# Kernel optimization log

Measured on AMD Instinct MI355X. Metric: run time of the kernel, lower is better.

## Reference

```python
import jax, jax.numpy as jnp
import numpy as np


def _elu_plus_one(x):
    # F.elu(x) + 1 == exp(x) for x<0, x+1 for x>=0
    return jnp.where(x > 0, x + 1.0, jnp.exp(jnp.minimum(x, 0.0)))


def setup_inputs() -> dict:
    key = jax.random.key(0)
    kq, kk, kv = jax.random.split(key, 3)
    B, N, D = 16, 8192, 64
    q = jax.random.normal(kq, (B, N, D), dtype=jnp.float32)
    k = jax.random.normal(kk, (B, N, D), dtype=jnp.float32)
    v = jax.random.normal(kv, (B, N, D), dtype=jnp.float32)
    return {"q": q, "k": k, "v": v}


def reference(q, k, v):
    # linear attention with elu+1 feature map:
    # out = phi(q) @ (phi(k)^T @ v) / (D * N)
    qf = _elu_plus_one(q)          # [B, N, D]
    kf = _elu_plus_one(k)          # [B, N, D]
    kv = jnp.einsum('bnd,bne->bde', kf, v)   # [B, D, D] small intermediate
    denom = jnp.asarray(v.shape[-1] * v.shape[-2], dtype=v.dtype)
    out = jnp.einsum('bnd,bde->bne', qf, kv) / denom  # [B, N, D]
    return out
```

## Files before the change

### kernel.cpp

```cpp
#include <hip/hip_runtime.h>

#define B_ 16
#define N_ 8192
#define D_ 64

__device__ __forceinline__ float elu1(float x) {
    return x > 0.0f ? x + 1.0f : __expf(x);
}

__global__ __launch_bounds__(256, 4) void k1_partial(const float* __restrict__ kin,
                                                     const float* __restrict__ vin,
                                                     float* __restrict__ part,
                                                     int C, int R) {
    const int bid = blockIdx.x;
    const int b = bid / C, c = bid % C;
    const int w = threadIdx.x >> 6;
    const int lane = threadIdx.x & 63;
    const int dq = lane >> 3;
    const int eq = lane & 7;

    const int rows_per_wave = R >> 2;
    const size_t row0 = (size_t)b * N_ + (size_t)c * R + (size_t)w * rows_per_wave;
    const float* kbase = kin + row0 * D_ + 8 * dq;
    const float* vbase = vin + row0 * D_ + 8 * eq;

    float acc[8][8];
#pragma unroll
    for (int i = 0; i < 8; ++i)
#pragma unroll
        for (int jj = 0; jj < 8; ++jj) acc[i][jj] = 0.0f;

    for (int r = 0; r < rows_per_wave; r += 2) {
        const float4 ka0 = *(const float4*)(kbase + (size_t)(r + 0) * D_);
        const float4 kb0 = *(const float4*)(kbase + (size_t)(r + 0) * D_ + 4);
        const float4 va0 = *(const float4*)(vbase + (size_t)(r + 0) * D_);
        const float4 vb0 = *(const float4*)(vbase + (size_t)(r + 0) * D_ + 4);
        const float4 ka1 = *(const float4*)(kbase + (size_t)(r + 1) * D_);
        const float4 kb1 = *(const float4*)(kbase + (size_t)(r + 1) * D_ + 4);
        const float4 va1 = *(const float4*)(vbase + (size_t)(r + 1) * D_);
        const float4 vb1 = *(const float4*)(vbase + (size_t)(r + 1) * D_ + 4);

        const float kk0[8] = {elu1(ka0.x), elu1(ka0.y), elu1(ka0.z), elu1(ka0.w),
                              elu1(kb0.x), elu1(kb0.y), elu1(kb0.z), elu1(kb0.w)};
        const float vv0[8] = {va0.x, va0.y, va0.z, va0.w, vb0.x, vb0.y, vb0.z, vb0.w};
#pragma unroll
        for (int i = 0; i < 8; ++i)
#pragma unroll
            for (int jj = 0; jj < 8; ++jj)
                acc[i][jj] = __fmaf_rn(kk0[i], vv0[jj], acc[i][jj]);

        const float kk1[8] = {elu1(ka1.x), elu1(ka1.y), elu1(ka1.z), elu1(ka1.w),
                              elu1(kb1.x), elu1(kb1.y), elu1(kb1.z), elu1(kb1.w)};
        const float vv1[8] = {va1.x, va1.y, va1.z, va1.w, vb1.x, vb1.y, vb1.z, vb1.w};
#pragma unroll
        for (int i = 0; i < 8; ++i)
#pragma unroll
            for (int jj = 0; jj < 8; ++jj)
                acc[i][jj] = __fmaf_rn(kk1[i], vv1[jj], acc[i][jj]);
    }

    __shared__ float red[D_ * D_];
    for (int ww = 0; ww < 4; ++ww) {
        if (w == ww) {
#pragma unroll
            for (int i = 0; i < 8; ++i)
#pragma unroll
                for (int jq = 0; jq < 2; ++jq) {
                    float* p = &red[(8 * dq + i) * D_ + 8 * eq + 4 * jq];
                    if (ww == 0) {
                        float4 o = {acc[i][4 * jq + 0], acc[i][4 * jq + 1],
                                    acc[i][4 * jq + 2], acc[i][4 * jq + 3]};
                        *(float4*)p = o;
                    } else {
                        float4 cur = *(const float4*)p;
                        float4 o = {cur.x + acc[i][4 * jq + 0], cur.y + acc[i][4 * jq + 1],
                                    cur.z + acc[i][4 * jq + 2], cur.w + acc[i][4 * jq + 3]};
                        *(float4*)p = o;
                    }
                }
        }
        __syncthreads();
    }

    float4* pb = (float4*)(part + (size_t)bid * (D_ * D_));
    const float4* rp = (const float4*)red;
#pragma unroll
    for (int u = 0; u < 4; ++u)
        pb[threadIdx.x + 256 * u] = rp[threadIdx.x + 256 * u];
}

template <int TI>
__global__ __launch_bounds__(256) void k1_atomic(const float* __restrict__ kin,
                                                 const float* __restrict__ vin,
                                                 float* __restrict__ kv,
                                                 int C, int R) {
    const int bid = blockIdx.x;
    const int b = bid / C, c = bid % C;
    const size_t base = ((size_t)b * N_ + (size_t)c * R) * D_;
    const float4* kp = (const float4*)(kin + base);
    const float4* vp = (const float4*)(vin + base);

    __shared__ float lk[TI][D_];
    __shared__ float lv[TI][D_];

    const int tid = threadIdx.x;
    const int td = tid >> 4;
    const int te = tid & 15;

    float acc[4][4];
#pragma unroll
    for (int i = 0; i < 4; ++i)
#pragma unroll
        for (int j = 0; j < 4; ++j) acc[i][j] = 0.0f;

    const int ntiles = R / TI;
    for (int t = 0; t < ntiles; ++t) {
#pragma unroll
        for (int u = tid; u < TI * (D_ / 4); u += 256) {
            float4 kk = kp[t * TI * (D_ / 4) + u];
            float4 vv = vp[t * TI * (D_ / 4) + u];
            const int r = u >> 4, cc = (u & 15) * 4;
            float4 ek;
            ek.x = elu1(kk.x); ek.y = elu1(kk.y);
            ek.z = elu1(kk.z); ek.w = elu1(kk.w);
            *(float4*)&lk[r][cc] = ek;
            *(float4*)&lv[r][cc] = vv;
        }
        __syncthreads();
#pragma unroll 8
        for (int r = 0; r < TI; ++r) {
            const float4 kk = *(const float4*)&lk[r][td * 4];
            const float4 vv = *(const float4*)&lv[r][te * 4];
            const float kd[4] = {kk.x, kk.y, kk.z, kk.w};
            const float ve[4] = {vv.x, vv.y, vv.z, vv.w};
#pragma unroll
            for (int i = 0; i < 4; ++i)
#pragma unroll
                for (int j = 0; j < 4; ++j)
                    acc[i][j] = __fmaf_rn(kd[i], ve[j], acc[i][j]);
        }
        __syncthreads();
    }

    float* pb = kv + (size_t)b * (D_ * D_);
#pragma unroll
    for (int i = 0; i < 4; ++i)
#pragma unroll
        for (int j = 0; j < 4; ++j)
            atomicAdd(&pb[(4 * td + i) * D_ + 4 * te + j], acc[i][j]);
}

__global__ __launch_bounds__(256) void k2_reduce(float* __restrict__ part, int C) {
    const int i = blockIdx.x * 256 + threadIdx.x;
    const int b = i >> 12, jj = i & 4095;
    float* p = part + (size_t)b * C * (D_ * D_) + jj;
    float s0 = 0.0f, s1 = 0.0f, s2 = 0.0f, s3 = 0.0f;
    int c = 0;
    for (; c + 4 <= C; c += 4) {
        s0 += p[(size_t)(c + 0) * (D_ * D_)];
        s1 += p[(size_t)(c + 1) * (D_ * D_)];
        s2 += p[(size_t)(c + 2) * (D_ * D_)];
        s3 += p[(size_t)(c + 3) * (D_ * D_)];
    }
    for (; c < C; ++c) s0 += p[(size_t)c * (D_ * D_)];
    p[0] = (s0 + s1) + (s2 + s3);
}

__global__ __launch_bounds__(256, 4) void k3_out(const float* __restrict__ q,
                                                 const float* __restrict__ kvbuf,
                                                 int kvstride,
                                                 float* __restrict__ out) {
    __shared__ float skv[D_ * D_];
    const int b = blockIdx.x >> 7;
    const int tile = blockIdx.x & 127;

    const float4* kvg = (const float4*)(kvbuf + (size_t)b * kvstride);
    float4* skv4 = (float4*)skv;
#pragma unroll
    for (int u = 0; u < 4; ++u)
        skv4[threadIdx.x + 256 * u] = kvg[threadIdx.x + 256 * u];

    const int r = threadIdx.x >> 2;
    const int j = threadIdx.x & 3;
    const size_t row = (size_t)b * N_ + (size_t)tile * 64 + r;

    const float4* qp = (const float4*)(q + row * D_ + j * 16);
    float qf[16];
#pragma unroll
    for (int u = 0; u < 4; ++u) {
        float4 t = qp[u];
        qf[4 * u + 0] = elu1(t.x);
        qf[4 * u + 1] = elu1(t.y);
        qf[4 * u + 2] = elu1(t.z);
        qf[4 * u + 3] = elu1(t.w);
    }
    __syncthreads();

    float4 acc[4];
#pragma unroll
    for (int s = 0; s < 4; ++s) acc[s] = {0.0f, 0.0f, 0.0f, 0.0f};

    for (int d0 = 0; d0 < 4; ++d0) {
        const int dbase = d0 * 16;
#pragma unroll
        for (int dd = 0; dd < 16; ++dd) {
            const float qd = __shfl(qf[dd], d0, 4);
            const int d = dbase + dd;
#pragma unroll
            for (int s = 0; s < 4; ++s) {
                const float4 kvv = *(const float4*)&skv[d * D_ + s * 16 + j * 4];
                acc[s].x = __fmaf_rn(qd, kvv.x, acc[s].x);
                acc[s].y = __fmaf_rn(qd, kvv.y, acc[s].y);
                acc[s].z = __fmaf_rn(qd, kvv.z, acc[s].z);
                acc[s].w = __fmaf_rn(qd, kvv.w, acc[s].w);
            }
        }
    }

    const float scale = 1.0f / (float)((size_t)D_ * N_);
    float4* op = (float4*)(out + row * D_);
#pragma unroll
    for (int s = 0; s < 4; ++s) {
        float4 o = {acc[s].x * scale, acc[s].y * scale,
                    acc[s].z * scale, acc[s].w * scale};
        op[s * 4 + j] = o;
    }
}

extern "C" void kernel_launch(void* const* d_in, const int* in_sizes, int n_in,
                              void* d_out, int out_size, void* d_ws, size_t ws_size,
                              hipStream_t stream) {
    const float* q = (const float*)d_in[0];
    const float* k = (const float*)d_in[1];
    const float* v = (const float*)d_in[2];
    float* out = (float*)d_out;
    float* ws = (float*)d_ws;

    const size_t mat = (size_t)D_ * D_;

    int C = 0;
    for (int cc = 64; cc >= 2; cc >>= 1) {
        if (ws_size >= (size_t)B_ * cc * mat * sizeof(float)) { C = cc; break; }
    }

    if (C >= 2) {
        const int R = N_ / C;
        k1_partial<<<B_ * C, 256, 0, stream>>>(k, v, ws, C, R);
        k2_reduce<<<(int)(B_ * mat) / 256, 256, 0, stream>>>(ws, C);
        k3_out<<<B_ * (N_ / 64), 256, 0, stream>>>(q, ws, (int)(C * mat), out);
    } else {
        hipMemsetAsync(d_ws, 0, B_ * mat * sizeof(float), stream);
        const int C2 = 64, R = N_ / C2;
        k1_atomic<32><<<B_ * C2, 256, 0, stream>>>(k, v, ws, C2, R);
        k3_out<<<B_ * (N_ / 64), 256, 0, stream>>>(q, ws, (int)mat, out);
    }
}
```

Before: 172.2 us.

## Compute two output rows per thread in k3 and raise partial-split cap

```diff
diff --git a/kernel.cpp b/kernel.cpp
--- a/kernel.cpp
+++ b/kernel.cpp
@@ -171,8 +171,8 @@
                                                  int kvstride,
                                                  float* __restrict__ out) {
     __shared__ float skv[D_ * D_];
-    const int b = blockIdx.x >> 7;
-    const int tile = blockIdx.x & 127;
+    const int b = blockIdx.x >> 6;
+    const int tile = blockIdx.x & 63;
 
     const float4* kvg = (const float4*)(kvbuf + (size_t)b * kvstride);
     float4* skv4 = (float4*)skv;
@@ -180,50 +180,63 @@
     for (int u = 0; u < 4; ++u)
         skv4[threadIdx.x + 256 * u] = kvg[threadIdx.x + 256 * u];
 
-    const int r = threadIdx.x >> 2;
+    const int rp = threadIdx.x >> 2;
     const int j = threadIdx.x & 3;
-    const size_t row = (size_t)b * N_ + (size_t)tile * 64 + r;
-
-    const float4* qp = (const float4*)(q + row * D_ + j * 16);
-    float qf[16];
-#pragma unroll
-    for (int u = 0; u < 4; ++u) {
-        float4 t = qp[u];
-        qf[4 * u + 0] = elu1(t.x);
-        qf[4 * u + 1] = elu1(t.y);
-        qf[4 * u + 2] = elu1(t.z);
-        qf[4 * u + 3] = elu1(t.w);
-    }
+    const size_t row0 = (size_t)b * N_ + (size_t)tile * 128 + 2 * rp;
+    const float* q0 = q + row0 * D_;
+    const float* q1 = q0 + D_;
+
     __syncthreads();
 
-    float4 acc[4];
-#pragma unroll
-    for (int s = 0; s < 4; ++s) acc[s] = {0.0f, 0.0f, 0.0f, 0.0f};
+    float4 acc0[4], acc1[4];
+#pragma unroll
+    for (int s = 0; s < 4; ++s) {
+        acc0[s] = {0.0f, 0.0f, 0.0f, 0.0f};
+        acc1[s] = {0.0f, 0.0f, 0.0f, 0.0f};
+    }
 
     for (int d0 = 0; d0 < 4; ++d0) {
-        const int dbase = d0 * 16;
+        float qa[16], qb[16];
+#pragma unroll
+        for (int u = 0; u < 4; ++u) {
+            float4 ta = *(const float4*)(q0 + d0 * 16 + 4 * u);
+            float4 tb = *(const float4*)(q1 + d0 * 16 + 4 * u);
+            qa[4 * u + 0] = elu1(ta.x); qa[4 * u + 1] = elu1(ta.y);
+            qa[4 * u + 2] = elu1(ta.z); qa[4 * u + 3] = elu1(ta.w);
+            qb[4 * u + 0] = elu1(tb.x); qb[4 * u + 1] = elu1(tb.y);
+            qb[4 * u + 2] = elu1(tb.z); qb[4 * u + 3] = elu1(tb.w);
+        }
 #pragma unroll
         for (int dd = 0; dd < 16; ++dd) {
-            const float qd = __shfl(qf[dd], d0, 4);
-            const int d = dbase + dd;
+            const int d = d0 * 16 + dd;
+            const float qda = qa[dd];
+            const float qdb = qb[dd];
 #pragma unroll
             for (int s = 0; s < 4; ++s) {
                 const float4 kvv = *(const float4*)&skv[d * D_ + s * 16 + j * 4];
-                acc[s].x = __fmaf_rn(qd, kvv.x, acc[s].x);
-                acc[s].y = __fmaf_rn(qd, kvv.y, acc[s].y);
-                acc[s].z = __fmaf_rn(qd, kvv.z, acc[s].z);
-                acc[s].w = __fmaf_rn(qd, kvv.w, acc[s].w);
+                acc0[s].x = __fmaf_rn(qda, kvv.x, acc0[s].x);
+                acc0[s].y = __fmaf_rn(qda, kvv.y, acc0[s].y);
+                acc0[s].z = __fmaf_rn(qda, kvv.z, acc0[s].z);
+                acc0[s].w = __fmaf_rn(qda, kvv.w, acc0[s].w);
+                acc1[s].x = __fmaf_rn(qdb, kvv.x, acc1[s].x);
+                acc1[s].y = __fmaf_rn(qdb, kvv.y, acc1[s].y);
+                acc1[s].z = __fmaf_rn(qdb, kvv.z, acc1[s].z);
+                acc1[s].w = __fmaf_rn(qdb, kvv.w, acc1[s].w);
             }
         }
     }
 
     const float scale = 1.0f / (float)((size_t)D_ * N_);
-    float4* op = (float4*)(out + row * D_);
+    float4* op0 = (float4*)(out + row0 * D_);
+    float4* op1 = (float4*)(out + (row0 + 1) * D_);
 #pragma unroll
     for (int s = 0; s < 4; ++s) {
-        float4 o = {acc[s].x * scale, acc[s].y * scale,
-                    acc[s].z * scale, acc[s].w * scale};
-        op[s * 4 + j] = o;
+        float4 o0 = {acc0[s].x * scale, acc0[s].y * scale,
+                     acc0[s].z * scale, acc0[s].w * scale};
+        float4 o1 = {acc1[s].x * scale, acc1[s].y * scale,
+                     acc1[s].z * scale, acc1[s].w * scale};
+        op0[4 * s + j] = o0;
+        op1[4 * s + j] = o1;
     }
 }
 
@@ -239,7 +252,7 @@
     const size_t mat = (size_t)D_ * D_;
 
     int C = 0;
-    for (int cc = 64; cc >= 2; cc >>= 1) {
+    for (int cc = 128; cc >= 2; cc >>= 1) {
         if (ws_size >= (size_t)B_ * cc * mat * sizeof(float)) { C = cc; break; }
     }
 
@@ -247,11 +260,11 @@
         const int R = N_ / C;
         k1_partial<<<B_ * C, 256, 0, stream>>>(k, v, ws, C, R);
         k2_reduce<<<(int)(B_ * mat) / 256, 256, 0, stream>>>(ws, C);
-        k3_out<<<B_ * (N_ / 64), 256, 0, stream>>>(q, ws, (int)(C * mat), out);
+        k3_out<<<B_ * (N_ / 128), 256, 0, stream>>>(q, ws, (int)(C * mat), out);
     } else {
         hipMemsetAsync(d_ws, 0, B_ * mat * sizeof(float), stream);
         const int C2 = 64, R = N_ / C2;
         k1_atomic<32><<<B_ * C2, 256, 0, stream>>>(k, v, ws, C2, R);
-        k3_out<<<B_ * (N_ / 64), 256, 0, stream>>>(q, ws, (int)mat, out);
-    }
-}
+        k3_out<<<B_ * (N_ / 128), 256, 0, stream>>>(q, ws, (int)mat, out);
+    }
+}
```

Result: no change. 174.0 us (+1.0%).
